# Kernel tuning notes

Measured on AMD Instinct MI355X. Metric: run time of the kernel, lower is better.

## Reference

```python
import jax, jax.numpy as jnp
import numpy as np

DIM = 1024
NUM_HEADS = 16
HEAD_DIM = DIM // NUM_HEADS
ROPE_BASE = 10000.0


def apply_rope(x, pos):
    """x: [B, H, N, D] float32, pos: [B, N] int -> rotated x (rotate-half convention)."""
    d = x.shape[-1]
    # inv_freq: [D/2]
    inv_freq = 1.0 / (ROPE_BASE ** (jnp.arange(0, d, 2, dtype=jnp.float32) / d))
    # angles: [B, 1, N, D/2]
    ang = pos.astype(jnp.float32)[:, None, :, None] * inv_freq
    cos = jnp.concatenate([jnp.cos(ang), jnp.cos(ang)], axis=-1)
    sin = jnp.concatenate([jnp.sin(ang), jnp.sin(ang)], axis=-1)
    x1, x2 = x[..., : d // 2], x[..., d // 2 :]
    rotated = jnp.concatenate([-x2, x1], axis=-1)
    return x * cos + rotated * sin


def setup_inputs() -> dict:
    key = jax.random.key(0)
    ks = jax.random.split(key, 10)
    B, Nq, Nk, C = 4, 512, 2048, DIM
    scale = 0.02
    inp = {
        "query": jax.random.normal(ks[0], (B, Nq, C), dtype=jnp.float32),
        "key": jax.random.normal(ks[1], (B, Nk, C), dtype=jnp.float32),
        "value": jax.random.normal(ks[2], (B, Nk, C), dtype=jnp.float32),
        "qpos": jnp.sort(jax.random.randint(ks[3], (B, Nq), 0, Nk, dtype=jnp.int32), axis=-1),
        "kpos": jnp.sort(jax.random.randint(ks[4], (B, Nk), 0, Nk, dtype=jnp.int32), axis=-1),
        # learned params (qkv_bias=False; output proj has bias, per nn.Linear default)
        "Wq": jax.random.normal(ks[5], (C, C), dtype=jnp.float32) * scale,
        "Wk": jax.random.normal(ks[6], (C, C), dtype=jnp.float32) * scale,
        "Wv": jax.random.normal(ks[7], (C, C), dtype=jnp.float32) * scale,
        "Wp": jax.random.normal(ks[8], (C, C), dtype=jnp.float32) * scale,
        "bp": jax.random.normal(ks[9], (C,), dtype=jnp.float32) * scale,
    }
    return inp


def reference(query, key, value, qpos, kpos, Wq, Wk, Wv, Wp, bp):
    B, Nq, C = query.shape
    Nk = key.shape[1]
    H, D = NUM_HEADS, C // NUM_HEADS
    scale = D ** (-0.5)

    # separate Q/K/V linear projections (bias=False), split heads -> [B, H, N, D]
    q = (query @ Wq.T).reshape(B, Nq, H, D).transpose(0, 2, 1, 3)
    k = (key @ Wk.T).reshape(B, Nk, H, D).transpose(0, 2, 1, 3)
    v = (value @ Wv.T).reshape(B, Nk, H, D).transpose(0, 2, 1, 3)

    # RoPE applied in fp32 (matches the cast-to-float/rotate/cast-back sequence)
    q = apply_rope(q.astype(jnp.float32), qpos).astype(query.dtype)
    k = apply_rope(k.astype(jnp.float32), kpos).astype(key.dtype)

    # scaled dot-product attention (dropout_p = 0.0, non-causal)
    scores = jnp.einsum("bhqd,bhkd->bhqk", q, k) * scale
    attn = jax.nn.softmax(scores, axis=-1)
    x = jnp.einsum("bhqk,bhkd->bhqd", attn, v)

    # merge heads and output projection (with bias)
    x = x.transpose(0, 2, 1, 3).reshape(B, Nq, C)
    x = x @ Wp.T + bp
    return x
```

## Files before the change

### kernel.cpp

```cpp
#include <hip/hip_runtime.h>
#include <math.h>

#define B_ 4
#define NQ 512
#define NK 2048
#define C_ 1024
#define H_ 16
#define D_ 64
#define KK 1024

typedef __attribute__((ext_vector_type(8))) _Float16 half8;
typedef __attribute__((ext_vector_type(4))) _Float16 half4;
typedef __attribute__((ext_vector_type(4))) float float4v;

__device__ __forceinline__ void g2l16(const _Float16* g, _Float16* l)
{
    __builtin_amdgcn_global_load_lds(
        (const __attribute__((address_space(1))) unsigned int*)g,
        (__attribute__((address_space(3))) unsigned int*)l, 16, 0, 0);
}

__global__ __launch_bounds__(256) void cvt_w_tab(const float* __restrict__ W0,
                                                 const float* __restrict__ W1,
                                                 const float* __restrict__ W2,
                                                 const float* __restrict__ W3,
                                                 _Float16* __restrict__ W16,
                                                 float2* __restrict__ tab)
{
    const int blk = blockIdx.x;
    if (blk < 4096) {
        const int w = blk >> 10, row = blk & 1023;
        const float* src = (w == 0) ? W0 : (w == 1) ? W1 : (w == 2) ? W2 : W3;
        const int col = threadIdx.x * 4;
        float4 f = *(const float4*)(src + (size_t)row * 1024 + col);
        half4 h;
        h[0] = (_Float16)f.x; h[1] = (_Float16)f.y;
        h[2] = (_Float16)f.z; h[3] = (_Float16)f.w;
        *(half4*)(W16 + ((size_t)w << 20) + (size_t)row * 1024 + col) = h;
        return;
    }
    const int idx = (blk - 4096) * 256 + threadIdx.x;
    const int p = idx >> 5, i = idx & 31;

    double f = 1.0;
    if (i & 1)  f *= 0.7498942093324559;
    if (i & 2)  f *= 0.5623413251903491;
    if (i & 4)  f *= 0.31622776601683794;
    if (i & 8)  f *= 0.1;
    if (i & 16) f *= 0.01;

    const double ang = (double)p * f;
    const double TWO_PI = 6.2831853071795864769;
    const double INV_TWO_PI = 0.15915494309189533577;
    const float red = (float)(ang - TWO_PI * floor(ang * INV_TWO_PI));
    float s, c;
    sincosf(red, &s, &c);
    tab[idx] = make_float2(c, s);
}

__global__ __launch_bounds__(256) void gemm_proj(const float* __restrict__ qf,
                                                 const float* __restrict__ kf,
                                                 const float* __restrict__ vf,
                                                 const _Float16* __restrict__ W16,
                                                 const int* __restrict__ qpos,
                                                 const int* __restrict__ kpos,
                                                 const float2* __restrict__ tab,
                                                 _Float16* __restrict__ qhp,
                                                 _Float16* __restrict__ khp,
                                                 _Float16* __restrict__ vtp)
{
    __shared__ _Float16 sA[128 * 64];
    __shared__ _Float16 sB[128 * 64];

    const int lbid = blockIdx.x;
    const int xcd = lbid & 7;
    const int seq = lbid >> 3;
    const int y = xcd + 8 * (seq >> 3);
    const int n0 = (seq & 7) * 128;

    const float* A; const _Float16* Bw; _Float16* Yh; const int* pos;
    int nsh, m0, mode; float scale;
    if (y < 64)       { A = kf; Bw = W16 + (1u << 20); Yh = khp; pos = kpos; nsh = 11; m0 = y * 128;         mode = 0; scale = 1.0f; }
    else if (y < 128) { A = vf; Bw = W16 + (2u << 20); Yh = vtp; pos = nullptr; nsh = 11; m0 = (y - 64) * 128;  mode = 2; scale = 0.0f; }
    else              { A = qf; Bw = W16;              Yh = qhp; pos = qpos; nsh = 9;  m0 = (y - 128) * 128; mode = 0; scale = 0.125f; }

    const int tid = threadIdx.x;
    const int lane = tid & 63, wave = tid >> 6;
    const int wm = (wave >> 1) * 64, wn = (wave & 1) * 64;
    const int fm = lane & 15, quad = lane >> 4;

    const int r0 = lane >> 3;
    const int c4 = lane & 7;
    const int sc = c4 ^ r0;
    const float*    gAl = A  + (size_t)(m0 + wave * 32 + r0) * KK + sc * 8;
    const _Float16* gB  = Bw + (size_t)(n0 + wave * 32 + r0) * KK + sc * 8;

    float4v acc[4][4];
    #pragma unroll
    for (int i = 0; i < 4; ++i)
        #pragma unroll
        for (int j = 0; j < 4; ++j)
            #pragma unroll
            for (int e = 0; e < 4; ++e) acc[i][j][e] = 0.0f;

    float4 va[8];
    #pragma unroll
    for (int u = 0; u < 4; ++u) {
        va[2 * u]     = *(const float4*)(gAl + (size_t)u * 8 * KK);
        va[2 * u + 1] = *(const float4*)(gAl + (size_t)u * 8 * KK + 4);
    }

    for (int k0 = 0; k0 < KK; k0 += 64) {
        __syncthreads();
        #pragma unroll
        for (int u = 0; u < 4; ++u) {
            half8 h;
            h[0] = (_Float16)va[2 * u].x; h[1] = (_Float16)va[2 * u].y;
            h[2] = (_Float16)va[2 * u].z; h[3] = (_Float16)va[2 * u].w;
            h[4] = (_Float16)va[2 * u + 1].x; h[5] = (_Float16)va[2 * u + 1].y;
            h[6] = (_Float16)va[2 * u + 1].z; h[7] = (_Float16)va[2 * u + 1].w;
            *(half8*)&sA[(wave * 32 + u * 8 + r0) * 64 + c4 * 8] = h;
        }
        #pragma unroll
        for (int u = 0; u < 4; ++u)
            g2l16(gB + (size_t)u * 8 * KK + k0, &sB[(wave * 32 + u * 8) * 64]);
        __syncthreads();

        if (k0 + 64 < KK) {
            #pragma unroll
            for (int u = 0; u < 4; ++u) {
                va[2 * u]     = *(const float4*)(gAl + (size_t)u * 8 * KK + k0 + 64);
                va[2 * u + 1] = *(const float4*)(gAl + (size_t)u * 8 * KK + k0 + 68);
            }
        }

        #pragma unroll
        for (int ks = 0; ks < 2; ++ks) {
            const int po = ((ks * 4 + quad) ^ (fm & 7)) * 8;
            half8 a[4], b[4];
            #pragma unroll
            for (int i = 0; i < 4; ++i) {
                a[i] = *(const half8*)&sA[(wm + i * 16 + fm) * 64 + po];
                b[i] = *(const half8*)&sB[(wn + i * 16 + fm) * 64 + po];
            }
            __builtin_amdgcn_s_setprio(1);
            #pragma unroll
            for (int i = 0; i < 4; ++i)
                #pragma unroll
                for (int j = 0; j < 4; ++j)
                    acc[i][j] = __builtin_amdgcn_mfma_f32_16x16x32_f16(a[i], b[j], acc[i][j], 0, 0, 0);
            __builtin_amdgcn_s_setprio(0);
        }
    }

    const int rr = quad * 4;
    if (mode == 0) {
        const int nmask = (1 << nsh) - 1;
        const int hidx = (n0 + wn) >> 6;
        #pragma unroll
        for (int i = 0; i < 4; ++i)
            #pragma unroll
            for (int r = 0; r < 4; ++r) {
                const int m = m0 + wm + i * 16 + rr + r;
                const int b = m >> nsh, n = m & nmask;
                const int p = pos[(b << nsh) + n];
                const float2 cs0 = tab[p * 32 + fm];
                const float2 cs1 = tab[p * 32 + 16 + fm];
                const float x0 = acc[i][0][r], x2 = acc[i][2][r];
                const float x1 = acc[i][1][r], x3 = acc[i][3][r];
                const float o0 = (x0 * cs0.x - x2 * cs0.y) * scale;
                const float o2 = (x2 * cs0.x + x0 * cs0.y) * scale;
                const float o1 = (x1 * cs1.x - x3 * cs1.y) * scale;
                const float o3 = (x3 * cs1.x + x1 * cs1.y) * scale;
                const size_t base = ((((size_t)b * H_ + hidx) << nsh) + n) * 64 + fm;
                Yh[base +  0] = (_Float16)o0;
                Yh[base + 16] = (_Float16)o1;
                Yh[base + 32] = (_Float16)o2;
                Yh[base + 48] = (_Float16)o3;
            }
    } else {
        const int nmask = (1 << nsh) - 1;
        #pragma unroll
        for (int i = 0; i < 4; ++i)
            #pragma unroll
            for (int r = 0; r < 4; ++r) {
                const int m = m0 + wm + i * 16 + rr + r;
                const int b = m >> nsh, n = m & nmask;
                #pragma unroll
                for (int j = 0; j < 4; ++j) {
                    const int c = n0 + wn + j * 16 + fm;
                    Yh[(((size_t)(b * H_ + (c >> 6)) * 64) + (c & 63)) * NK + n] = (_Float16)acc[i][j][r];
                }
            }
    }
}

__global__ __launch_bounds__(256) void gemm_out(const _Float16* __restrict__ A,
                                                const _Float16* __restrict__ Bw,
                                                float* __restrict__ Yf,
                                                const float* __restrict__ bias)
{
    __shared__ _Float16 sA[128 * 64];
    __shared__ _Float16 sB[128 * 64];

    const int tid = threadIdx.x;
    const int lane = tid & 63, wave = tid >> 6;
    const int n0 = blockIdx.x * 128, m0 = blockIdx.y * 128;
    const int wm = (wave >> 1) * 64, wn = (wave & 1) * 64;
    const int fm = lane & 15, quad = lane >> 4;

    const int srow = wave * 32 + (lane >> 3);
    const int soct = (lane & 7) ^ (srow & 7);
    const _Float16* gA = A  + (size_t)(m0 + srow) * KK + soct * 8;
    const _Float16* gB = Bw + (size_t)(n0 + srow) * KK + soct * 8;

    float4v acc[4][4];
    #pragma unroll
    for (int i = 0; i < 4; ++i)
        #pragma unroll
        for (int j = 0; j < 4; ++j)
            #pragma unroll
            for (int e = 0; e < 4; ++e) acc[i][j][e] = 0.0f;

    for (int k0 = 0; k0 < KK; k0 += 64) {
        __syncthreads();
        #pragma unroll
        for (int u = 0; u < 4; ++u) {
            g2l16(gA + (size_t)u * 8 * KK + k0, &sA[(wave * 32 + u * 8) * 64]);
            g2l16(gB + (size_t)u * 8 * KK + k0, &sB[(wave * 32 + u * 8) * 64]);
        }
        __syncthreads();

        #pragma unroll
        for (int ks = 0; ks < 2; ++ks) {
            const int po = ((ks * 4 + quad) ^ (fm & 7)) * 8;
            half8 a[4], b[4];
            #pragma unroll
            for (int i = 0; i < 4; ++i) {
                a[i] = *(const half8*)&sA[(wm + i * 16 + fm) * 64 + po];
                b[i] = *(const half8*)&sB[(wn + i * 16 + fm) * 64 + po];
            }
            __builtin_amdgcn_s_setprio(1);
            #pragma unroll
            for (int i = 0; i < 4; ++i)
                #pragma unroll
                for (int j = 0; j < 4; ++j)
                    acc[i][j] = __builtin_amdgcn_mfma_f32_16x16x32_f16(a[i], b[j], acc[i][j], 0, 0, 0);
            __builtin_amdgcn_s_setprio(0);
        }
    }

    const int rr = quad * 4;
    #pragma unroll
    for (int i = 0; i < 4; ++i)
        #pragma unroll
        for (int r = 0; r < 4; ++r) {
            const int m = m0 + wm + i * 16 + rr + r;
            #pragma unroll
            for (int j = 0; j < 4; ++j) {
                const int c = n0 + wn + j * 16 + fm;
                Yf[(size_t)m * 1024 + c] = acc[i][j][r] + bias[c];
            }
        }
}

__global__ __launch_bounds__(512) void attn_fused(const _Float16* __restrict__ qh,
                                                  const _Float16* __restrict__ kh,
                                                  const _Float16* __restrict__ vt,
                                                  _Float16* __restrict__ xw16)
{
    __shared__ _Float16 sK[2][64 * 64];
    __shared__ _Float16 sV[2][64 * 64];
    __shared__ _Float16 ps[8][16][66];

    const int tid = threadIdx.x;
    const int lane = tid & 63, wv = tid >> 6;
    const int bhi = blockIdx.x & 63;
    const int qquad = blockIdx.x >> 6;
    const size_t bh = (size_t)bhi;
    const int qt = qquad * 8 + wv;

    const int fm = lane & 15;
    const int quad = lane >> 4;
    const int fq = quad * 8;

    const _Float16* kb = kh + bh * NK * 64;
    const _Float16* vb = vt + bh * (size_t)64 * NK;

    const int r0 = lane >> 3;
    const int c4 = lane & 7;
    const int sch = c4 ^ r0;
    const _Float16* gK = kb + (size_t)(wv * 8 + r0) * 64 + sch * 8;
    const _Float16* gV = vb + (size_t)(wv * 8 + r0) * NK + sch * 8;

    const _Float16* qb = qh + (bh * NQ + (size_t)qt * 16) * 64;
    half8 aq[2];
    aq[0] = *(const half8*)(qb + (size_t)fm * 64 + fq);
    aq[1] = *(const half8*)(qb + (size_t)fm * 64 + 32 + fq);

    float l_acc[4] = {};
    float4v O[4];
    #pragma unroll
    for (int j = 0; j < 4; ++j)
        #pragma unroll
        for (int e = 0; e < 4; ++e) O[j][e] = 0.0f;

    const float4v z4 = {0.0f, 0.0f, 0.0f, 0.0f};

    g2l16(gK, &sK[0][wv * 512]);
    g2l16(gV, &sV[0][wv * 512]);
    __syncthreads();

    for (int it = 0; it < 32; ++it) {
        const int cur = it & 1;
        if (it < 31) {
            g2l16(gK + (size_t)(it + 1) * 64 * 64, &sK[cur ^ 1][wv * 512]);
            g2l16(gV + (it + 1) * 64,              &sV[cur ^ 1][wv * 512]);
        }
        const _Float16* Kc = sK[cur];
        const _Float16* Vc = sV[cur];

        half8 bk[4][2];
        #pragma unroll
        for (int j = 0; j < 4; ++j)
            #pragma unroll
            for (int ks = 0; ks < 2; ++ks)
                bk[j][ks] = *(const half8*)&Kc[(j * 16 + fm) * 64 + (((ks * 4 + quad) ^ (fm & 7)) * 8)];

        float4v s[4];
        __builtin_amdgcn_s_setprio(1);
        #pragma unroll
        for (int j = 0; j < 4; ++j) {
            s[j] = __builtin_amdgcn_mfma_f32_16x16x32_f16(aq[0], bk[j][0], z4, 0, 0, 0);
            s[j] = __builtin_amdgcn_mfma_f32_16x16x32_f16(aq[1], bk[j][1], s[j], 0, 0, 0);
        }
        __builtin_amdgcn_s_setprio(0);

        half8 bv[4][2];
        #pragma unroll
        for (int j = 0; j < 4; ++j)
            #pragma unroll
            for (int ks = 0; ks < 2; ++ks)
                bv[j][ks] = *(const half8*)&Vc[(j * 16 + fm) * 64 + (((ks * 4 + quad) ^ (fm & 7)) * 8)];

        #pragma unroll
        for (int j = 0; j < 4; ++j)
            #pragma unroll
            for (int r = 0; r < 4; ++r) {
                const float p = __expf(s[j][r]);
                l_acc[r] += p;
                ps[wv][quad * 4 + r][16 * j + fm] = (_Float16)p;
            }

        __builtin_amdgcn_s_setprio(1);
        #pragma unroll
        for (int ks = 0; ks < 2; ++ks) {
            half8 pa = *(const half8*)&ps[wv][fm][ks * 32 + fq];
            #pragma unroll
            for (int j = 0; j < 4; ++j)
                O[j] = __builtin_amdgcn_mfma_f32_16x16x32_f16(pa, bv[j][ks], O[j], 0, 0, 0);
        }
        __builtin_amdgcn_s_setprio(0);

        __syncthreads();
    }

    #pragma unroll
    for (int r = 0; r < 4; ++r) {
        float l = l_acc[r];
        l += __shfl_xor(l, 1);
        l += __shfl_xor(l, 2);
        l += __shfl_xor(l, 4);
        l += __shfl_xor(l, 8);
        const float inv = 1.0f / l;
        const int qr = quad * 4 + r;
        const int row = (bhi >> 4) * 512 + qt * 16 + qr;
        #pragma unroll
        for (int j = 0; j < 4; ++j) {
            const int col = (bhi & 15) * 64 + j * 16 + fm;
            xw16[(size_t)row * 1024 + col] = (_Float16)(O[j][r] * inv);
        }
    }
}

extern "C" void kernel_launch(void* const* d_in, const int* in_sizes, int n_in,
                              void* d_out, int out_size, void* d_ws, size_t ws_size,
                              hipStream_t stream)
{
    const float* query = (const float*)d_in[0];
    const float* key   = (const float*)d_in[1];
    const float* value = (const float*)d_in[2];
    const int*   qpos  = (const int*)d_in[3];
    const int*   kpos  = (const int*)d_in[4];
    const float* Wq    = (const float*)d_in[5];
    const float* Wk    = (const float*)d_in[6];
    const float* Wv    = (const float*)d_in[7];
    const float* Wp    = (const float*)d_in[8];
    const float* bp    = (const float*)d_in[9];
    float* out = (float*)d_out;

    char* ws = (char*)d_ws;
    float2*   tab   = (float2*)  (ws);
    _Float16* xw16  = (_Float16*)(ws + (32u << 20));
    _Float16* W16   = (_Float16*)(ws + (36u << 20));
    _Float16* qhp   = (_Float16*)(ws + (44u << 20));
    _Float16* khp   = (_Float16*)(ws + (48u << 20));
    _Float16* vtp   = (_Float16*)(ws + (64u << 20));

    cvt_w_tab<<<4352, 256, 0, stream>>>(Wq, Wk, Wv, Wp, W16, tab);

    gemm_proj<<<1152, 256, 0, stream>>>(query, key, value, W16, qpos, kpos, tab,
                                        qhp, khp, vtp);

    attn_fused<<<256, 512, 0, stream>>>(qhp, khp, vtp, xw16);

    gemm_out<<<dim3(8, 16), 256, 0, stream>>>(xw16, W16 + (3u << 20), out, bp);
}
```

Before: 274.1 us.

## Pre-convert Q/K/V activations to fp16 and load GEMM A tiles via direct-to-LDS

```diff
diff --git a/kernel.cpp b/kernel.cpp
--- a/kernel.cpp
+++ b/kernel.cpp
@@ -20,54 +20,67 @@
         (__attribute__((address_space(3))) unsigned int*)l, 16, 0, 0);
 }
 
-__global__ __launch_bounds__(256) void cvt_w_tab(const float* __restrict__ W0,
-                                                 const float* __restrict__ W1,
-                                                 const float* __restrict__ W2,
-                                                 const float* __restrict__ W3,
-                                                 _Float16* __restrict__ W16,
-                                                 float2* __restrict__ tab)
+__global__ __launch_bounds__(256) void cvt_all(const float* __restrict__ W0,
+                                               const float* __restrict__ W1,
+                                               const float* __restrict__ W2,
+                                               const float* __restrict__ W3,
+                                               const float* __restrict__ q,
+                                               const float* __restrict__ k,
+                                               const float* __restrict__ v,
+                                               _Float16* __restrict__ W16,
+                                               _Float16* __restrict__ xq,
+                                               _Float16* __restrict__ xk,
+                                               _Float16* __restrict__ xv,
+                                               float2* __restrict__ tab)
 {
     const int blk = blockIdx.x;
+    if (blk >= 22528) {
+        const int idx = (blk - 22528) * 256 + threadIdx.x;
+        const int p = idx >> 5, i = idx & 31;
+        double f = 1.0;
+        if (i & 1)  f *= 0.7498942093324559;
+        if (i & 2)  f *= 0.5623413251903491;
+        if (i & 4)  f *= 0.31622776601683794;
+        if (i & 8)  f *= 0.1;
+        if (i & 16) f *= 0.01;
+        const double ang = (double)p * f;
+        const double TWO_PI = 6.2831853071795864769;
+        const double INV_TWO_PI = 0.15915494309189533577;
+        const float red = (float)(ang - TWO_PI * floor(ang * INV_TWO_PI));
+        float s, c;
+        sincosf(red, &s, &c);
+        tab[idx] = make_float2(c, s);
+        return;
+    }
+    const float* src; _Float16* dst; int row;
     if (blk < 4096) {
-        const int w = blk >> 10, row = blk & 1023;
-        const float* src = (w == 0) ? W0 : (w == 1) ? W1 : (w == 2) ? W2 : W3;
-        const int col = threadIdx.x * 4;
-        float4 f = *(const float4*)(src + (size_t)row * 1024 + col);
-        half4 h;
-        h[0] = (_Float16)f.x; h[1] = (_Float16)f.y;
-        h[2] = (_Float16)f.z; h[3] = (_Float16)f.w;
-        *(half4*)(W16 + ((size_t)w << 20) + (size_t)row * 1024 + col) = h;
-        return;
-    }
-    const int idx = (blk - 4096) * 256 + threadIdx.x;
-    const int p = idx >> 5, i = idx & 31;
-
-    double f = 1.0;
-    if (i & 1)  f *= 0.7498942093324559;
-    if (i & 2)  f *= 0.5623413251903491;
-    if (i & 4)  f *= 0.31622776601683794;
-    if (i & 8)  f *= 0.1;
-    if (i & 16) f *= 0.01;
-
-    const double ang = (double)p * f;
-    const double TWO_PI = 6.2831853071795864769;
-    const double INV_TWO_PI = 0.15915494309189533577;
-    const float red = (float)(ang - TWO_PI * floor(ang * INV_TWO_PI));
-    float s, c;
-    sincosf(red, &s, &c);
-    tab[idx] = make_float2(c, s);
-}
-
-__global__ __launch_bounds__(256) void gemm_proj(const float* __restrict__ qf,
-                                                 const float* __restrict__ kf,
-                                                 const float* __restrict__ vf,
-                                                 const _Float16* __restrict__ W16,
-                                                 const int* __restrict__ qpos,
-                                                 const int* __restrict__ kpos,
-                                                 const float2* __restrict__ tab,
-                                                 _Float16* __restrict__ qhp,
-                                                 _Float16* __restrict__ khp,
-                                                 _Float16* __restrict__ vtp)
+        const int w = blk >> 10; row = blk & 1023;
+        src = (w == 0) ? W0 : (w == 1) ? W1 : (w == 2) ? W2 : W3;
+        dst = W16 + ((size_t)w << 20);
+    } else {
+        const int b2 = blk - 4096;
+        if (b2 < 2048)       { src = q; dst = xq; row = b2; }
+        else if (b2 < 10240) { src = k; dst = xk; row = b2 - 2048; }
+        else                 { src = v; dst = xv; row = b2 - 10240; }
+    }
+    const int col = threadIdx.x * 4;
+    float4 f = *(const float4*)(src + (size_t)row * 1024 + col);
+    half4 h;
+    h[0] = (_Float16)f.x; h[1] = (_Float16)f.y;
+    h[2] = (_Float16)f.z; h[3] = (_Float16)f.w;
+    *(half4*)(dst + (size_t)row * 1024 + col) = h;
+}
+
+__global__ __launch_bounds__(256) void gemm_qkv(const _Float16* __restrict__ xq,
+                                                const _Float16* __restrict__ xk,
+                                                const _Float16* __restrict__ xv,
+                                                const _Float16* __restrict__ W16,
+                                                const int* __restrict__ qpos,
+                                                const int* __restrict__ kpos,
+                                                const float2* __restrict__ tab,
+                                                _Float16* __restrict__ qhp,
+                                                _Float16* __restrict__ khp,
+                                                _Float16* __restrict__ vtp)
 {
     __shared__ _Float16 sA[128 * 64];
     __shared__ _Float16 sB[128 * 64];
@@ -78,22 +91,21 @@
     const int y = xcd + 8 * (seq >> 3);
     const int n0 = (seq & 7) * 128;
 
-    const float* A; const _Float16* Bw; _Float16* Yh; const int* pos;
+    const _Float16* A; const _Float16* Bw; _Float16* Yh; const int* pos;
     int nsh, m0, mode; float scale;
-    if (y < 64)       { A = kf; Bw = W16 + (1u << 20); Yh = khp; pos = kpos; nsh = 11; m0 = y * 128;         mode = 0; scale = 1.0f; }
-    else if (y < 128) { A = vf; Bw = W16 + (2u << 20); Yh = vtp; pos = nullptr; nsh = 11; m0 = (y - 64) * 128;  mode = 2; scale = 0.0f; }
-    else              { A = qf; Bw = W16;              Yh = qhp; pos = qpos; nsh = 9;  m0 = (y - 128) * 128; mode = 0; scale = 0.125f; }
+    if (y < 64)       { A = xk; Bw = W16 + (1u << 20); Yh = khp; pos = kpos;   nsh = 11; m0 = y * 128;         mode = 0; scale = 1.0f;   }
+    else if (y < 128) { A = xv; Bw = W16 + (2u << 20); Yh = vtp; pos = nullptr; nsh = 11; m0 = (y - 64) * 128;  mode = 2; scale = 0.0f;   }
+    else              { A = xq; Bw = W16;              Yh = qhp; pos = qpos;   nsh = 9;  m0 = (y - 128) * 128; mode = 0; scale = 0.125f; }
 
     const int tid = threadIdx.x;
     const int lane = tid & 63, wave = tid >> 6;
     const int wm = (wave >> 1) * 64, wn = (wave & 1) * 64;
     const int fm = lane & 15, quad = lane >> 4;
 
-    const int r0 = lane >> 3;
-    const int c4 = lane & 7;
-    const int sc = c4 ^ r0;
-    const float*    gAl = A  + (size_t)(m0 + wave * 32 + r0) * KK + sc * 8;
-    const _Float16* gB  = Bw + (size_t)(n0 + wave * 32 + r0) * KK + sc * 8;
+    const int srow = wave * 32 + (lane >> 3);
+    const int soct = (lane & 7) ^ (srow & 7);
+    const _Float16* gA = A  + (size_t)(m0 + srow) * KK + soct * 8;
+    const _Float16* gB = Bw + (size_t)(n0 + srow) * KK + soct * 8;
 
     float4v acc[4][4];
     #pragma unroll
@@ -103,36 +115,14 @@
             #pragma unroll
             for (int e = 0; e < 4; ++e) acc[i][j][e] = 0.0f;
 
-    float4 va[8];
-    #pragma unroll
-    for (int u = 0; u < 4; ++u) {
-        va[2 * u]     = *(const float4*)(gAl + (size_t)u * 8 * KK);
-        va[2 * u + 1] = *(const float4*)(gAl + (size_t)u * 8 * KK + 4);
-    }
-
     for (int k0 = 0; k0 < KK; k0 += 64) {
         __syncthreads();
         #pragma unroll
         for (int u = 0; u < 4; ++u) {
-            half8 h;
-            h[0] = (_Float16)va[2 * u].x; h[1] = (_Float16)va[2 * u].y;
-            h[2] = (_Float16)va[2 * u].z; h[3] = (_Float16)va[2 * u].w;
-            h[4] = (_Float16)va[2 * u + 1].x; h[5] = (_Float16)va[2 * u + 1].y;
-            h[6] = (_Float16)va[2 * u + 1].z; h[7] = (_Float16)va[2 * u + 1].w;
-            *(half8*)&sA[(wave * 32 + u * 8 + r0) * 64 + c4 * 8] = h;
-        }
-        #pragma unroll
-        for (int u = 0; u < 4; ++u)
+            g2l16(gA + (size_t)u * 8 * KK + k0, &sA[(wave * 32 + u * 8) * 64]);
             g2l16(gB + (size_t)u * 8 * KK + k0, &sB[(wave * 32 + u * 8) * 64]);
+        }
         __syncthreads();
-
-        if (k0 + 64 < KK) {
-            #pragma unroll
-            for (int u = 0; u < 4; ++u) {
-                va[2 * u]     = *(const float4*)(gAl + (size_t)u * 8 * KK + k0 + 64);
-                va[2 * u + 1] = *(const float4*)(gAl + (size_t)u * 8 * KK + k0 + 68);
-            }
-        }
 
         #pragma unroll
         for (int ks = 0; ks < 2; ++ks) {
@@ -400,19 +390,22 @@
     float* out = (float*)d_out;
 
     char* ws = (char*)d_ws;
-    float2*   tab   = (float2*)  (ws);
-    _Float16* xw16  = (_Float16*)(ws + (32u << 20));
+    _Float16* xk16  = (_Float16*)(ws);
+    _Float16* xv16  = (_Float16*)(ws + (16u << 20));
+    _Float16* xq16  = (_Float16*)(ws + (32u << 20));
     _Float16* W16   = (_Float16*)(ws + (36u << 20));
     _Float16* qhp   = (_Float16*)(ws + (44u << 20));
     _Float16* khp   = (_Float16*)(ws + (48u << 20));
     _Float16* vtp   = (_Float16*)(ws + (64u << 20));
-
-    cvt_w_tab<<<4352, 256, 0, stream>>>(Wq, Wk, Wv, Wp, W16, tab);
-
-    gemm_proj<<<1152, 256, 0, stream>>>(query, key, value, W16, qpos, kpos, tab,
-                                        qhp, khp, vtp);
-
-    attn_fused<<<256, 512, 0, stream>>>(qhp, khp, vtp, xw16);
-
-    gemm_out<<<dim3(8, 16), 256, 0, stream>>>(xw16, W16 + (3u << 20), out, bp);
-}
+    float2*   tab   = (float2*)d_out;
+
+    cvt_all<<<22784, 256, 0, stream>>>(Wq, Wk, Wv, Wp, query, key, value,
+                                       W16, xq16, xk16, xv16, tab);
+
+    gemm_qkv<<<1152, 256, 0, stream>>>(xq16, xk16, xv16, W16, qpos, kpos, tab,
+                                       qhp, khp, vtp);
+
+    attn_fused<<<256, 512, 0, stream>>>(qhp, khp, vtp, xq16);
+
+    gemm_out<<<dim3(8, 16), 256, 0, stream>>>(xq16, W16 + (3u << 20), out, bp);
+}
```

Result: no change. 271.3 us (-1.0%).
